# Performance work log

Measured on AMD Instinct MI355X. Metric: run time of the kernel, lower is better.

The kernel has to match this reference:

```python
import jax, jax.numpy as jnp
import numpy as np

VOCAB, E, H, OUT = 50000, 300, 512, 256
D = 2 * H  # bidirectional
B, T = 64, 256
EPS = 1e-5


def setup_inputs() -> dict:
    key = jax.random.key(0)
    ks = jax.random.split(key, 16)
    s = 0.05
    inp = {
        'inputs': jax.random.randint(ks[0], (B, T), 0, VOCAB, dtype=jnp.int32),
        'mask': jnp.zeros((B, T), dtype=bool),
        'embed_table': jax.random.normal(ks[1], (VOCAB, E), jnp.float32) * s,
        # forward-direction LSTM (PyTorch gate order i,f,g,o)
        'w_ih_f': jax.random.normal(ks[2], (4 * H, E), jnp.float32) * s,
        'w_hh_f': jax.random.normal(ks[3], (4 * H, H), jnp.float32) * s,
        'b_ih_f': jax.random.normal(ks[4], (4 * H,), jnp.float32) * s,
        'b_hh_f': jax.random.normal(ks[5], (4 * H,), jnp.float32) * s,
        # backward-direction LSTM
        'w_ih_b': jax.random.normal(ks[6], (4 * H, E), jnp.float32) * s,
        'w_hh_b': jax.random.normal(ks[7], (4 * H, H), jnp.float32) * s,
        'b_ih_b': jax.random.normal(ks[8], (4 * H,), jnp.float32) * s,
        'b_hh_b': jax.random.normal(ks[9], (4 * H,), jnp.float32) * s,
        # SoftDotAttention
        'w_in': jax.random.normal(ks[10], (D, D), jnp.float32) * s,       # linear_in, no bias
        'w_out_attn': jax.random.normal(ks[11], (D, 2 * D), jnp.float32) * s,  # linear_out, no bias
        # output head + BatchNorm affine
        'w_out': jax.random.normal(ks[12], (OUT, D), jnp.float32) * s,
        'b_out': jax.random.normal(ks[13], (OUT,), jnp.float32) * s,
        'gamma': jnp.ones((OUT,), jnp.float32),
        'beta': jnp.zeros((OUT,), jnp.float32),
    }
    return inp


def _lstm_dir(x, w_ih, w_hh, b_ih, b_hh, reverse):
    # x: [B, T, E] -> hs: [B, T, H]
    bsz = x.shape[0]
    h0 = jnp.zeros((bsz, w_hh.shape[1]), x.dtype)
    c0 = jnp.zeros_like(h0)
    x_pre = jnp.einsum('bte,ge->btg', x, w_ih) + (b_ih + b_hh)  # precompute input proj

    def cell(carry, xt):
        h, c = carry
        gates = xt + h @ w_hh.T
        i, f, g, o = jnp.split(gates, 4, axis=-1)
        i, f, o = jax.nn.sigmoid(i), jax.nn.sigmoid(f), jax.nn.sigmoid(o)
        g = jnp.tanh(g)
        c = f * c + i * g
        h = o * jnp.tanh(c)
        return (h, c), h

    _, hs = jax.lax.scan(cell, (h0, c0), jnp.swapaxes(x_pre, 0, 1), reverse=reverse)
    return jnp.swapaxes(hs, 0, 1)


def reference(inputs, mask, embed_table, w_ih_f, w_hh_f, b_ih_f, b_hh_f,
              w_ih_b, w_hh_b, b_ih_b, b_hh_b, w_in, w_out_attn,
              w_out, b_out, gamma, beta):
    embeds = embed_table[inputs]                       # [B,T,E]; dropout = identity (eval)
    h_f = _lstm_dir(embeds, w_ih_f, w_hh_f, b_ih_f, b_hh_f, reverse=False)
    h_b = _lstm_dir(embeds, w_ih_b, w_hh_b, b_ih_b, b_hh_b, reverse=True)
    ctx = jnp.concatenate([h_f, h_b], axis=-1)         # [B,T,D]

    # vectorized SoftDotAttention over all query timesteps (the original Python loop)
    target = jnp.einsum('bqd,ed->bqe', ctx, w_in)      # linear_in(ctx[:,q])
    scores = jnp.einsum('bqd,bkd->bqk', target, ctx)   # [B,T,T]
    scores = jnp.where(mask[:, None, :], -jnp.inf, scores)
    attn = jax.nn.softmax(scores, axis=-1)
    weighted = jnp.einsum('bqk,bkd->bqd', attn, ctx)   # [B,T,D]
    h_tilde = jnp.tanh(jnp.einsum('bqc,dc->bqd',
                                  jnp.concatenate([weighted, ctx], axis=-1),
                                  w_out_attn))          # [B,T,D]

    ctx_out = jnp.mean(h_tilde, axis=1)                # [B,D]
    y = jnp.tanh(ctx_out @ w_out.T + b_out)            # [B,OUT]

    # BatchNorm1d, training-mode batch statistics (biased variance)
    mu = jnp.mean(y, axis=0)
    var = jnp.mean((y - mu) ** 2, axis=0)
    out = gamma * (y - mu) * jax.lax.rsqrt(var + EPS) + beta
    return out
```

## Files before the change

kernel.cpp:

```cpp
#include <hip/hip_runtime.h>
#include <hip/hip_fp16.h>

#define NB   64
#define NT   256
#define NE   300
#define NH   512
#define ND   1024
#define NOUT 256

typedef _Float16 f16;
typedef _Float16 f16x4 __attribute__((ext_vector_type(4)));
typedef _Float16 f16x8 __attribute__((ext_vector_type(8)));
typedef float    f32x4 __attribute__((ext_vector_type(4)));

static __device__ __forceinline__ float sigmoidf_(float x) {
  return 1.f / (1.f + __expf(-x));
}
static __device__ __forceinline__ float tanhf_(float x) {
  return 1.f - 2.f / (__expf(2.f * x) + 1.f);
}

static __device__ __forceinline__ void gload16(const f16* g, f16* l) {
  __builtin_amdgcn_global_load_lds(
      (const __attribute__((address_space(1))) void*)g,
      (__attribute__((address_space(3))) void*)l, 16, 0, 0);
}

template <bool DUAL>
static __device__ __forceinline__ void mfma_tile128(
    const f16* __restrict__ A, const f16* __restrict__ A2,
    const f16* __restrict__ B, int K, int Ksplit, int ldA, int ldB,
    int m0, int n0, f32x4 acc[4][4], f16* As, f16* Bs)
{
  const int tid = threadIdx.x;
  const int lane = tid & 63, w = tid >> 6;
  const int wr = (w >> 1) * 64, wc = (w & 1) * 64;
  const int srow = w * 16 + (lane >> 2);
  const int scol = (lane & 3) * 8;
  const f16* A0  = A + (size_t)(m0 + srow) * ldA + scol;
  const f16* A1  = A + (size_t)(m0 + 64 + srow) * ldA + scol;
  const f16* A20 = DUAL ? (A2 + (size_t)(m0 + srow) * ldA + scol) : A0;
  const f16* A21 = DUAL ? (A2 + (size_t)(m0 + 64 + srow) * ldA + scol) : A1;
  const f16* B0  = B + (size_t)(n0 + srow) * ldB + scol;
  const f16* B1  = B + (size_t)(n0 + 64 + srow) * ldB + scol;
  f16* Asw0 = As + w * 512;
  f16* Asw1 = As + 2048 + w * 512;
  f16* Bsw0 = Bs + w * 512;
  f16* Bsw1 = Bs + 2048 + w * 512;
  for (int kt = 0; kt < K; kt += 32) {
    if (!DUAL || kt < Ksplit) {
      gload16(A0 + kt, Asw0);
      gload16(A1 + kt, Asw1);
    } else {
      gload16(A20 + (kt - Ksplit), Asw0);
      gload16(A21 + (kt - Ksplit), Asw1);
    }
    gload16(B0 + kt, Bsw0);
    gload16(B1 + kt, Bsw1);
    __syncthreads();
    f16x8 af[4], bf[4];
#pragma unroll
    for (int i = 0; i < 4; ++i) {
      af[i] = *(const f16x8*)&As[(wr + i * 16 + (lane & 15)) * 32 + (lane >> 4) * 8];
      bf[i] = *(const f16x8*)&Bs[(wc + i * 16 + (lane & 15)) * 32 + (lane >> 4) * 8];
    }
#pragma unroll
    for (int i = 0; i < 4; ++i)
#pragma unroll
      for (int j = 0; j < 4; ++j)
        acc[i][j] = __builtin_amdgcn_mfma_f32_16x16x32_f16(
            af[i], bf[j], acc[i][j], 0, 0, 0);
    __syncthreads();
  }
}

__global__ __launch_bounds__(256) void gemm128_h2h(
    const f16* __restrict__ A, const f16* __restrict__ B, f16* __restrict__ C,
    int N, int K, int sA, int sB, int sC)
{
  __shared__ __align__(16) f16 As[4096], Bs[4096];
  const f16* Ab = A + (size_t)blockIdx.z * sA;
  const f16* Bb = B + (size_t)blockIdx.z * sB;
  f16*       Cb = C + (size_t)blockIdx.z * sC;
  const int m0 = blockIdx.y * 128, n0 = blockIdx.x * 128;
  f32x4 acc[4][4] = {};
  mfma_tile128<false>(Ab, Ab, Bb, K, K, K, K, m0, n0, acc, As, Bs);
  const int lane = threadIdx.x & 63, w = threadIdx.x >> 6;
  const int wr = (w >> 1) * 64, wc = (w & 1) * 64;
#pragma unroll
  for (int i = 0; i < 4; ++i) {
    const int row = m0 + wr + i * 16 + (lane >> 4) * 4;
#pragma unroll
    for (int j = 0; j < 4; ++j) {
      const int col = n0 + wc + j * 16 + (lane & 15);
#pragma unroll
      for (int r = 0; r < 4; ++r)
        Cb[(size_t)(row + r) * N + col] = (f16)acc[i][j][r];
    }
  }
}

__global__ __launch_bounds__(256) void gemm128_h2f(
    const f16* __restrict__ A, const f16* __restrict__ B, float* __restrict__ C,
    int N, int K, int sA, int sB, int sC)
{
  __shared__ __align__(16) f16 As[4096], Bs[4096];
  const f16* Ab = A + (size_t)blockIdx.z * sA;
  const f16* Bb = B + (size_t)blockIdx.z * sB;
  float*     Cb = C + (size_t)blockIdx.z * sC;
  const int m0 = blockIdx.y * 128, n0 = blockIdx.x * 128;
  f32x4 acc[4][4] = {};
  mfma_tile128<false>(Ab, Ab, Bb, K, K, K, K, m0, n0, acc, As, Bs);
  const int lane = threadIdx.x & 63, w = threadIdx.x >> 6;
  const int wr = (w >> 1) * 64, wc = (w & 1) * 64;
#pragma unroll
  for (int i = 0; i < 4; ++i) {
    const int row = m0 + wr + i * 16 + (lane >> 4) * 4;
#pragma unroll
    for (int j = 0; j < 4; ++j) {
      const int col = n0 + wc + j * 16 + (lane & 15);
#pragma unroll
      for (int r = 0; r < 4; ++r)
        Cb[(size_t)(row + r) * N + col] = acc[i][j][r];
    }
  }
}

__global__ __launch_bounds__(256) void xpre_mfma(
    const f16* __restrict__ A, const f16* __restrict__ B,
    const float* __restrict__ bihf, const float* __restrict__ bhhf,
    const float* __restrict__ bihb, const float* __restrict__ bhhb,
    f16* __restrict__ xq)
{
  __shared__ __align__(16) f16 As[2048], Bs[2048];
  __shared__ __align__(16) f16 ldsT[64 * 72];
  __shared__ float biasS[64];
  const int ds = blockIdx.x;
  const int dir = ds >> 5, slice = ds & 31;
  const int t0 = blockIdx.y;
  const int tid = threadIdx.x, lane = tid & 63, w = tid >> 6;
  if (tid < 64) {
    int row = dir * 2048 + (tid & 3) * 512 + slice * 16 + (tid >> 2);
    biasS[tid] = (row < 2048) ? (bihf[row] + bhhf[row])
                              : (bihb[row - 2048] + bhhb[row - 2048]);
  }
  const int srow = w * 16 + (lane >> 2);
  const int scol = (lane & 3) * 8;
  const f16* Ab = A + ((size_t)(srow * 256 + t0)) * 320 + scol;
  const int brow = dir * 2048 + (srow & 3) * 512 + slice * 16 + (srow >> 2);
  const f16* Bb = B + (size_t)brow * 320 + scol;
  f16* Asw = As + w * 512;
  f16* Bsw = Bs + w * 512;
  f32x4 acc[4] = {};
  for (int kt = 0; kt < 320; kt += 32) {
    gload16(Ab + kt, Asw);
    gload16(Bb + kt, Bsw);
    __syncthreads();
    f16x8 a = *(const f16x8*)&As[(w * 16 + (lane & 15)) * 32 + (lane >> 4) * 8];
#pragma unroll
    for (int j = 0; j < 4; ++j) {
      f16x8 b = *(const f16x8*)&Bs[(j * 16 + (lane & 15)) * 32 + (lane >> 4) * 8];
      acc[j] = __builtin_amdgcn_mfma_f32_16x16x32_f16(a, b, acc[j], 0, 0, 0);
    }
    __syncthreads();
  }
#pragma unroll
  for (int j = 0; j < 4; ++j) {
    const int cl = j * 16 + (lane & 15);
#pragma unroll
    for (int r = 0; r < 4; ++r) {
      int b = w * 16 + (lane >> 4) * 4 + r;
      ldsT[b * 72 + cl] = (f16)(acc[j][r] + biasS[cl]);
    }
  }
  __syncthreads();
  f16* base = xq + (((size_t)t0 * 2 + dir) * 32 + slice) * 4096;
#pragma unroll
  for (int p = 0; p < 2; ++p) {
    int e = tid + 256 * p;
    int b = e >> 3, q8 = (e & 7) * 8;
    *(uint4*)(base + b * 64 + q8) = *(const uint4*)&ldsT[b * 72 + q8];
  }
}

__global__ __launch_bounds__(256) void htilde_mfma(
    const f16* __restrict__ Wt, const f16* __restrict__ CTX,
    const f16* __restrict__ Wo, float* __restrict__ ctx_out)
{
  __shared__ __align__(16) f16 As[4096], Bs[4096];
  __shared__ float red[4][128];
  const int m0 = blockIdx.y * 128, n0 = blockIdx.x * 128;
  f32x4 acc[4][4] = {};
  mfma_tile128<true>(Wt, CTX, Wo, 2048, 1024, 1024, 2048, m0, n0, acc, As, Bs);
  const int lane = threadIdx.x & 63, w = threadIdx.x >> 6;
  const int wc = (w & 1) * 64;
#pragma unroll
  for (int j = 0; j < 4; ++j) {
    float s = 0.f;
#pragma unroll
    for (int i = 0; i < 4; ++i)
#pragma unroll
      for (int r = 0; r < 4; ++r) s += tanhf(acc[i][j][r]);
    s += __shfl_xor(s, 16, 64);
    s += __shfl_xor(s, 32, 64);
    if (lane < 16) red[w][wc + j * 16 + lane] = s;
  }
  __syncthreads();
  if (threadIdx.x < 128) {
    const int col = threadIdx.x;
    float s = (col < 64) ? (red[0][col] + red[2][col])
                         : (red[1][col] + red[3][col]);
    int b = m0 >> 8;
    atomicAdd(&ctx_out[(size_t)b * ND + n0 + col], s);
  }
}

__global__ __launch_bounds__(256, 1) void lstm_persist(
    const f16* __restrict__ xq, const float* __restrict__ whhf,
    const float* __restrict__ whhb, f16* __restrict__ hseq)
{
  __shared__ __align__(16) f16 hx[2][64][24];
  const int blk = blockIdx.x;
  const int dir = blk >> 5;
  const int slice = blk & 31;
  const int j0 = slice * 16;
  const float* whh = dir ? whhb : whhf;
  const int tid = threadIdx.x, lane = tid & 63, w = tid >> 6;
  const int jj = lane & 15, ko = (lane >> 4) * 8;

  f16x8 bf[4][16];
#pragma unroll
  for (int g = 0; g < 4; ++g)
#pragma unroll
    for (int kt = 0; kt < 16; ++kt) {
      const float* src = whh + (size_t)(g * NH + j0 + jj) * NH + kt * 32 + ko;
      float4 u0 = *(const float4*)src;
      float4 u1 = *(const float4*)(src + 4);
      f16x8 v;
      v[0] = (f16)u0.x; v[1] = (f16)u0.y; v[2] = (f16)u0.z; v[3] = (f16)u0.w;
      v[4] = (f16)u1.x; v[5] = (f16)u1.y; v[6] = (f16)u1.z; v[7] = (f16)u1.w;
      bf[g][kt] = v;
    }

  float c[4] = {0.f, 0.f, 0.f, 0.f};
  const int eb = tid >> 2, eg = tid & 3;
  const int aoff = (ko >> 4) * 1024 + (w * 16 + jj) * 16 + (ko & 8);

  float xg[4][4];
  auto ldxg = [&](int t) {
    const int tl = dir ? (NT - 1 - t) : t;
    const f16* base = xq + (((size_t)tl * 2 + dir) * 32 + slice) * 4096;
#pragma unroll
    for (int r = 0; r < 4; ++r) {
      const int b = w * 16 + (lane >> 4) * 4 + r;
      unsigned long long u = *(const unsigned long long*)(base + b * 64 + jj * 4);
      f16x4 x = __builtin_bit_cast(f16x4, u);
      xg[0][r] = (float)x[0];
      xg[1][r] = (float)x[1];
      xg[2][r] = (float)x[2];
      xg[3][r] = (float)x[3];
    }
  };
  ldxg(0);

  for (int t = 0; t < NT; ++t) {
    const int tt = dir ? (NT - 1 - t) : t;

    f32x4 acc[4] = {};
    if (t > 0) {
      const int ttp = dir ? (NT - t) : (t - 1);
      const f16* hp = hseq + ((size_t)ttp * 2 + dir) * 32768 + aoff;
      unsigned long long u0[16], u1[16];
#pragma unroll
      for (int kt = 0; kt < 16; ++kt) {
        u0[kt] = __hip_atomic_load(
            (const unsigned long long*)(hp + kt * 2048),
            __ATOMIC_RELAXED, __HIP_MEMORY_SCOPE_AGENT);
        u1[kt] = __hip_atomic_load(
            (const unsigned long long*)(hp + kt * 2048 + 4),
            __ATOMIC_RELAXED, __HIP_MEMORY_SCOPE_AGENT);
      }
      for (;;) {
        int nb = 0;
#pragma unroll
        for (int kt = 0; kt < 16; ++kt) {
          nb |= (unsigned)(u0[kt] >> 48) == 0xFFFFu;
          nb |= (unsigned)(u1[kt] >> 48) == 0xFFFFu;
        }
        if (!__any(nb)) break;
#pragma unroll
        for (int kt = 0; kt < 16; ++kt) {
          if ((unsigned)(u0[kt] >> 48) == 0xFFFFu)
            u0[kt] = __hip_atomic_load(
                (const unsigned long long*)(hp + kt * 2048),
                __ATOMIC_RELAXED, __HIP_MEMORY_SCOPE_AGENT);
          if ((unsigned)(u1[kt] >> 48) == 0xFFFFu)
            u1[kt] = __hip_atomic_load(
                (const unsigned long long*)(hp + kt * 2048 + 4),
                __ATOMIC_RELAXED, __HIP_MEMORY_SCOPE_AGENT);
        }
      }
#pragma unroll
      for (int kt = 0; kt < 16; ++kt) {
        f16x4 a0 = __builtin_bit_cast(f16x4, u0[kt]);
        f16x4 a1 = __builtin_bit_cast(f16x4, u1[kt]);
        f16x8 a = __builtin_shufflevector(a0, a1, 0, 1, 2, 3, 4, 5, 6, 7);
#pragma unroll
        for (int g = 0; g < 4; ++g)
          acc[g] = __builtin_amdgcn_mfma_f32_16x16x32_f16(a, bf[g][kt], acc[g], 0, 0, 0);
      }
    }
#pragma unroll
    for (int r = 0; r < 4; ++r) {
      float iv = sigmoidf_(acc[0][r] + xg[0][r]);
      float fv = sigmoidf_(acc[1][r] + xg[1][r]);
      float gv = tanhf_   (acc[2][r] + xg[2][r]);
      float ov = sigmoidf_(acc[3][r] + xg[3][r]);
      c[r] = fv * c[r] + iv * gv;
      float h = ov * tanhf_(c[r]);
      hx[t & 1][w * 16 + (lane >> 4) * 4 + r][jj] = (f16)h;
    }
    __syncthreads();
    f16x4 hv;
#pragma unroll
    for (int i = 0; i < 4; ++i) hv[i] = hx[t & 1][eb][eg * 4 + i];
    unsigned long long pu = __builtin_bit_cast(unsigned long long, hv);
    __hip_atomic_store(
        (unsigned long long*)(hseq + ((size_t)tt * 2 + dir) * 32768
                              + (size_t)slice * 1024 + eb * 16 + eg * 4),
        pu, __ATOMIC_RELAXED, __HIP_MEMORY_SCOPE_AGENT);
    if (t == NT - 1) break;
    ldxg(t + 1);
  }
}

__global__ __launch_bounds__(256) void fill_sent(unsigned long long* __restrict__ p)
{
  size_t i = (size_t)blockIdx.x * 1024 + threadIdx.x;
#pragma unroll
  for (int k = 0; k < 4; ++k)
    __hip_atomic_store(p + i + k * 256, 0xFFFFFFFFFFFFFFFFull,
                       __ATOMIC_RELAXED, __HIP_MEMORY_SCOPE_AGENT);
}

__global__ __launch_bounds__(256) void tr_k(
    const f16* __restrict__ hseq, f16* __restrict__ ctx, f16* __restrict__ ctxT)
{
  __shared__ __align__(16) f16 X[4][64][72];
  const int t0 = blockIdx.x * 64;
  const int dir = blockIdx.y;
  const int bg = blockIdx.z;
  const int tid = threadIdx.x;
  for (int ci = 0; ci < 8; ++ci) {
#pragma unroll
    for (int p = 0; p < 8; ++p) {
      int q = tid + 256 * p;
      int ti = q >> 5, rem = q & 31;
      int si = rem >> 3, s2 = rem & 7;
      int bi = s2 >> 1, jjh = (s2 & 1) * 8;
      const f16* src = hseq
          + (((size_t)(t0 + ti) * 2 + dir) * 32 + ci * 4 + si) * 1024
          + (bg * 4 + bi) * 16 + jjh;
      *(uint4*)&X[bi][ti][si * 16 + jjh] = *(const uint4*)src;
    }
    __syncthreads();
#pragma unroll
    for (int p = 0; p < 8; ++p) {
      int q = tid + 256 * p;
      int bi = q >> 9, rem = q & 511;
      int ti = rem >> 3, sub = (rem & 7) * 8;
      f16* dst = ctx + ((size_t)(bg * 4 + bi) * NT + t0 + ti) * ND
                 + dir * 512 + ci * 64 + sub;
      *(uint4*)dst = *(const uint4*)&X[bi][ti][sub];
    }
#pragma unroll
    for (int p = 0; p < 8; ++p) {
      int q = tid + 256 * p;
      int bi = q >> 9, rem = q & 511;
      int dl = rem >> 3, ts = (rem & 7) * 8;
      f16x8 v;
#pragma unroll
      for (int k = 0; k < 8; ++k) v[k] = X[bi][ts + k][dl];
      f16* dst = ctxT + ((size_t)(bg * 4 + bi) * ND + dir * 512 + ci * 64 + dl) * NT
                 + t0 + ts;
      *(f16x8*)dst = v;
    }
    __syncthreads();
  }
}

__global__ __launch_bounds__(256) void softmax_rows(
    const float* __restrict__ sc, f16* __restrict__ probs)
{
  const int row = blockIdx.x * 4 + (threadIdx.x >> 6);
  const int lane = threadIdx.x & 63;
  const float* p = sc + (size_t)row * NT;
  float4 v = *(const float4*)&p[lane * 4];
  float mx = fmaxf(fmaxf(v.x, v.y), fmaxf(v.z, v.w));
#pragma unroll
  for (int s = 32; s >= 1; s >>= 1) mx = fmaxf(mx, __shfl_xor(mx, s, 64));
  v.x = __expf(v.x - mx); v.y = __expf(v.y - mx);
  v.z = __expf(v.z - mx); v.w = __expf(v.w - mx);
  float sm = v.x + v.y + v.z + v.w;
#pragma unroll
  for (int s = 32; s >= 1; s >>= 1) sm += __shfl_xor(sm, s, 64);
  float inv = 1.f / sm;
  f16* q = probs + (size_t)row * NT + lane * 4;
  q[0] = (f16)(v.x * inv); q[1] = (f16)(v.y * inv);
  q[2] = (f16)(v.z * inv); q[3] = (f16)(v.w * inv);
}

__global__ __launch_bounds__(256) void head_k(
    const float* __restrict__ ctx_out, const float* __restrict__ w_out,
    const float* __restrict__ b_out, float* __restrict__ y)
{
  const int b = blockIdx.x;
  __shared__ float cl[ND];
#pragma unroll
  for (int l = 0; l < 4; ++l)
    cl[threadIdx.x + 256 * l] =
        ctx_out[(size_t)b * ND + threadIdx.x + 256 * l] * (1.f / (float)NT);
  __syncthreads();
  const int n = threadIdx.x;
  float acc = b_out[n];
  for (int k = 0; k < ND; k += 4) {
    float4 w = *(const float4*)&w_out[(size_t)n * ND + k];
    acc += cl[k] * w.x + cl[k + 1] * w.y + cl[k + 2] * w.z + cl[k + 3] * w.w;
  }
  y[b * NOUT + n] = tanhf(acc);
}

__global__ __launch_bounds__(64) void bn_k(
    const float* __restrict__ y, const float* __restrict__ gamma,
    const float* __restrict__ beta, float* __restrict__ out)
{
  const int n = blockIdx.x, b = threadIdx.x;
  float v = y[b * NOUT + n];
  float s = v, sq = v * v;
#pragma unroll
  for (int k = 32; k >= 1; k >>= 1) {
    s  += __shfl_xor(s, k, 64);
    sq += __shfl_xor(sq, k, 64);
  }
  float mu = s * (1.f / 64.f);
  float var = sq * (1.f / 64.f) - mu * mu;
  float r = rsqrtf(var + 1e-5f);
  out[b * NOUT + n] = gamma[n] * (v - mu) * r + beta[n];
}

__global__ __launch_bounds__(256) void zero_k(float4* __restrict__ p, int n4)
{
  int i = blockIdx.x * 256 + threadIdx.x;
  if (i < n4) p[i] = make_float4(0.f, 0.f, 0.f, 0.f);
}

__global__ __launch_bounds__(256) void gather_emb(
    const int* __restrict__ toks, const float* __restrict__ table,
    f16* __restrict__ emb)
{
  const int w = threadIdx.x >> 6, lane = threadIdx.x & 63;
  const int row = blockIdx.x * 4 + w;
  const int tok = toks[row];
  for (int k = lane; k < 320; k += 64)
    emb[(size_t)row * 320 + k] = (k < NE) ? (f16)table[(size_t)tok * NE + k]
                                          : (f16)0.f;
}

__global__ __launch_bounds__(256) void cvt_wih(
    const float* __restrict__ wf, const float* __restrict__ wb,
    f16* __restrict__ o)
{
  const int row = blockIdx.x;
  const float* src = (row < 2048) ? (wf + (size_t)row * NE)
                                  : (wb + (size_t)(row - 2048) * NE);
  for (int k = threadIdx.x; k < 320; k += 256)
    o[(size_t)row * 320 + k] = (k < NE) ? (f16)src[k] : (f16)0.f;
}

__global__ __launch_bounds__(256) void cvt_flat(
    const float* __restrict__ in, f16* __restrict__ o, int n)
{
  int i = blockIdx.x * 256 + threadIdx.x;
  if (i < n) o[i] = (f16)in[i];
}

extern "C" void kernel_launch(void* const* d_in, const int* in_sizes, int n_in,
                              void* d_out, int out_size, void* d_ws,
                              size_t ws_size, hipStream_t stream)
{
  (void)in_sizes; (void)n_in; (void)out_size;
  const int*   inputs  = (const int*)d_in[0];
  const float* table   = (const float*)d_in[2];
  const float* w_ih_f  = (const float*)d_in[3];
  const float* w_hh_f  = (const float*)d_in[4];
  const float* b_ih_f  = (const float*)d_in[5];
  const float* b_hh_f  = (const float*)d_in[6];
  const float* w_ih_b  = (const float*)d_in[7];
  const float* w_hh_b  = (const float*)d_in[8];
  const float* b_ih_b  = (const float*)d_in[9];
  const float* b_hh_b  = (const float*)d_in[10];
  const float* w_in    = (const float*)d_in[11];
  const float* w_oattn = (const float*)d_in[12];
  const float* w_out   = (const float*)d_in[13];
  const float* b_out   = (const float*)d_in[14];
  const float* gamma   = (const float*)d_in[15];
  const float* beta    = (const float*)d_in[16];

  char* ws = (char*)d_ws;
  f16*   xq      = (f16*)ws;
  f16*   ctxT_h  = (f16*)ws;
  f16*   tw_h    = (f16*)(ws + 33554432);
  float* scores  = (float*)(ws + 67108864);
  f16*   probs   = (f16*)(ws + 83886080);
  f16*   w_in_h  = (f16*)(ws + 92274688);
  f16*   ctx_h   = (f16*)(ws + 134217728);
  f16*   hseq    = (f16*)(ws + 167772160);
  f16*   emb_h   = (f16*)(ws + 201326592);
  float* ctxout  = (float*)(ws + 201588736);
  float* yb      = (float*)(ws + 201850880);
  f16*   wih_h   = (f16*)(ws + 211812352);
  f16*   w_oattn_h = (f16*)(ws + 214433792);
  if (ws_size < 218628096ULL) return;

  gather_emb<<<4096, 256, 0, stream>>>(inputs, table, emb_h);
  cvt_wih<<<4096, 256, 0, stream>>>(w_ih_f, w_ih_b, wih_h);
  cvt_flat<<<8192, 256, 0, stream>>>(w_oattn, w_oattn_h, 2097152);

  fill_sent<<<4096, 256, 0, stream>>>((unsigned long long*)hseq);

  xpre_mfma<<<dim3(64, 256), 256, 0, stream>>>(
      emb_h, wih_h, b_ih_f, b_hh_f, b_ih_b, b_hh_b, xq);

  zero_k<<<82, 256, 0, stream>>>((float4*)ctxout, 20992);
  lstm_persist<<<64, 256, 0, stream>>>(xq, w_hh_f, w_hh_b, hseq);

  tr_k<<<dim3(4, 2, 16), 256, 0, stream>>>(hseq, ctx_h, ctxT_h);

  cvt_flat<<<4096, 256, 0, stream>>>(w_in, w_in_h, 1048576);
  gemm128_h2h<<<dim3(8, 128, 1), 256, 0, stream>>>(
      ctx_h, w_in_h, tw_h, ND, ND, 0, 0, 0);

  gemm128_h2f<<<dim3(2, 2, NB), 256, 0, stream>>>(
      tw_h, ctx_h, scores, NT, ND, NT * ND, NT * ND, NT * NT);

  softmax_rows<<<(NB * NT) / 4, 256, 0, stream>>>(scores, probs);

  gemm128_h2h<<<dim3(8, 2, NB), 256, 0, stream>>>(
      probs, ctxT_h, tw_h, ND, NT, NT * NT, ND * NT, NT * ND);

  htilde_mfma<<<dim3(8, 128), 256, 0, stream>>>(tw_h, ctx_h, w_oattn_h, ctxout);

  head_k<<<NB, 256, 0, stream>>>(ctxout, w_out, b_out, yb);

  bn_k<<<NOUT, 64, 0, stream>>>(yb, gamma, beta, (float*)d_out);
}
```

Measured before the change: 1.559 ms.

## Enlarge xpre GEMM tile to 128x128 and merge prep kernels into one launch

The input-projection GEMM now gives each block two timesteps and two gate slices, a 128x128 tile, with a 4x4 MFMA accumulator per wave instead of 1x4. Each loaded operand fragment is reused across more MFMAs and the grid shrinks fourfold. Separately, the embedding gather, weight conversions and sentinel fill are fused into one prep kernel to cut launch overhead. The larger tile raises register and LDS use, which may lower occupancy.

```diff
diff --git a/kernel.cpp b/kernel.cpp
--- a/kernel.cpp
+++ b/kernel.cpp
@@ -132,54 +132,76 @@
     const float* __restrict__ bihb, const float* __restrict__ bhhb,
     f16* __restrict__ xq)
 {
-  __shared__ __align__(16) f16 As[2048], Bs[2048];
-  __shared__ __align__(16) f16 ldsT[64 * 72];
-  __shared__ float biasS[64];
-  const int ds = blockIdx.x;
-  const int dir = ds >> 5, slice = ds & 31;
-  const int t0 = blockIdx.y;
+  __shared__ __align__(16) f16 As[4096], Bs[4096];
+  __shared__ __align__(16) f16 ldsT[4][64][72];
+  __shared__ float biasS[128];
+  const int bx = blockIdx.x;
+  const int dir = bx >> 4, sp = bx & 15;
+  const int by = blockIdx.y;
   const int tid = threadIdx.x, lane = tid & 63, w = tid >> 6;
-  if (tid < 64) {
-    int row = dir * 2048 + (tid & 3) * 512 + slice * 16 + (tid >> 2);
-    biasS[tid] = (row < 2048) ? (bihf[row] + bhhf[row])
-                              : (bihb[row - 2048] + bhhb[row - 2048]);
-  }
-  const int srow = w * 16 + (lane >> 2);
+  if (tid < 128) {
+    int nc = tid & 63, soff = tid >> 6;
+    int rr = (nc & 3) * 512 + (sp * 2 + soff) * 16 + (nc >> 2);
+    biasS[tid] = dir ? (bihb[rr] + bhhb[rr]) : (bihf[rr] + bhhf[rr]);
+  }
+  const int s0 = w * 16 + (lane >> 2);
   const int scol = (lane & 3) * 8;
-  const f16* Ab = A + ((size_t)(srow * 256 + t0)) * 320 + scol;
-  const int brow = dir * 2048 + (srow & 3) * 512 + slice * 16 + (srow >> 2);
-  const f16* Bb = B + (size_t)brow * 320 + scol;
-  f16* Asw = As + w * 512;
-  f16* Bsw = Bs + w * 512;
-  f32x4 acc[4] = {};
+  const f16* A0 = A + ((size_t)s0 * 256 + 2 * by) * 320 + scol;
+  const f16* A1 = A0 + 320;
+  const int brow0 = dir * 2048 + (s0 & 3) * 512 + (sp * 2 + 0) * 16 + (s0 >> 2);
+  const int brow1 = dir * 2048 + (s0 & 3) * 512 + (sp * 2 + 1) * 16 + (s0 >> 2);
+  const f16* B0 = B + (size_t)brow0 * 320 + scol;
+  const f16* B1 = B + (size_t)brow1 * 320 + scol;
+  f16* Asw0 = As + w * 512;  f16* Asw1 = As + 2048 + w * 512;
+  f16* Bsw0 = Bs + w * 512;  f16* Bsw1 = Bs + 2048 + w * 512;
+  const int wr = (w >> 1) * 64, wc = (w & 1) * 64;
+  f32x4 acc[4][4] = {};
   for (int kt = 0; kt < 320; kt += 32) {
-    gload16(Ab + kt, Asw);
-    gload16(Bb + kt, Bsw);
-    __syncthreads();
-    f16x8 a = *(const f16x8*)&As[(w * 16 + (lane & 15)) * 32 + (lane >> 4) * 8];
-#pragma unroll
-    for (int j = 0; j < 4; ++j) {
-      f16x8 b = *(const f16x8*)&Bs[(j * 16 + (lane & 15)) * 32 + (lane >> 4) * 8];
-      acc[j] = __builtin_amdgcn_mfma_f32_16x16x32_f16(a, b, acc[j], 0, 0, 0);
-    }
+    gload16(A0 + kt, Asw0);
+    gload16(A1 + kt, Asw1);
+    gload16(B0 + kt, Bsw0);
+    gload16(B1 + kt, Bsw1);
+    __syncthreads();
+    f16x8 af[4], bf[4];
+#pragma unroll
+    for (int i = 0; i < 4; ++i) {
+      af[i] = *(const f16x8*)&As[(wr + i * 16 + (lane & 15)) * 32 + (lane >> 4) * 8];
+      bf[i] = *(const f16x8*)&Bs[(wc + i * 16 + (lane & 15)) * 32 + (lane >> 4) * 8];
+    }
+#pragma unroll
+    for (int i = 0; i < 4; ++i)
+#pragma unroll
+      for (int j = 0; j < 4; ++j)
+        acc[i][j] = __builtin_amdgcn_mfma_f32_16x16x32_f16(
+            af[i], bf[j], acc[i][j], 0, 0, 0);
     __syncthreads();
   }
 #pragma unroll
   for (int j = 0; j < 4; ++j) {
-    const int cl = j * 16 + (lane & 15);
-#pragma unroll
-    for (int r = 0; r < 4; ++r) {
-      int b = w * 16 + (lane >> 4) * 4 + r;
-      ldsT[b * 72 + cl] = (f16)(acc[j][r] + biasS[cl]);
+    const int n = wc + j * 16 + (lane & 15);
+    const int soff = n >> 6, nc = n & 63;
+    const float bias = biasS[n];
+#pragma unroll
+    for (int i = 0; i < 4; ++i) {
+#pragma unroll
+      for (int r = 0; r < 4; ++r) {
+        int row = wr + i * 16 + (lane >> 4) * 4 + r;
+        int dt = row >> 6, b = row & 63;
+        ldsT[dt * 2 + soff][b][nc] = (f16)(acc[i][j][r] + bias);
+      }
     }
   }
   __syncthreads();
-  f16* base = xq + (((size_t)t0 * 2 + dir) * 32 + slice) * 4096;
-#pragma unroll
-  for (int p = 0; p < 2; ++p) {
-    int e = tid + 256 * p;
-    int b = e >> 3, q8 = (e & 7) * 8;
-    *(uint4*)(base + b * 64 + q8) = *(const uint4*)&ldsT[b * 72 + q8];
+#pragma unroll
+  for (int sl = 0; sl < 4; ++sl) {
+    const int dt = sl >> 1, soff = sl & 1;
+    f16* base = xq + (((size_t)(2 * by + dt) * 2 + dir) * 32 + (sp * 2 + soff)) * 4096;
+#pragma unroll
+    for (int p = 0; p < 2; ++p) {
+      int e = tid + 256 * p;
+      int b = e >> 3, q8 = (e & 7) * 8;
+      *(uint4*)(base + b * 64 + q8) = *(const uint4*)&ldsT[sl][b][q8];
+    }
   }
 }
 
@@ -334,13 +356,61 @@
   }
 }
 
-__global__ __launch_bounds__(256) void fill_sent(unsigned long long* __restrict__ p)
-{
-  size_t i = (size_t)blockIdx.x * 1024 + threadIdx.x;
-#pragma unroll
-  for (int k = 0; k < 4; ++k)
-    __hip_atomic_store(p + i + k * 256, 0xFFFFFFFFFFFFFFFFull,
-                       __ATOMIC_RELAXED, __HIP_MEMORY_SCOPE_AGENT);
+__global__ __launch_bounds__(256) void prep_k(
+    const int* __restrict__ toks, const float* __restrict__ table,
+    f16* __restrict__ emb,
+    const float* __restrict__ wf, const float* __restrict__ wb,
+    f16* __restrict__ wih,
+    const float* __restrict__ woa, f16* __restrict__ woa_h,
+    unsigned long long* __restrict__ sent)
+{
+  int bb = blockIdx.x;
+  const int tid = threadIdx.x;
+  if (bb < 4096) {
+    const int w = tid >> 6, lane = tid & 63;
+    const int row = bb * 4 + w;
+    const int tok = toks[row];
+    for (int k = lane; k < 320; k += 64)
+      emb[(size_t)row * 320 + k] = (k < NE) ? (f16)table[(size_t)tok * NE + k]
+                                            : (f16)0.f;
+    return;
+  }
+  bb -= 4096;
+  if (bb < 4096) {
+    const int row = bb;
+    const float* src = (row < 2048) ? (wf + (size_t)row * NE)
+                                    : (wb + (size_t)(row - 2048) * NE);
+    for (int k = tid; k < 320; k += 256)
+      wih[(size_t)row * 320 + k] = (k < NE) ? (f16)src[k] : (f16)0.f;
+    return;
+  }
+  bb -= 4096;
+  if (bb < 8192) {
+    int i = bb * 256 + tid;
+    woa_h[i] = (f16)woa[i];
+    return;
+  }
+  bb -= 8192;
+  {
+    size_t i = (size_t)bb * 1024 + tid;
+#pragma unroll
+    for (int k = 0; k < 4; ++k)
+      __hip_atomic_store(sent + i + k * 256, 0xFFFFFFFFFFFFFFFFull,
+                         __ATOMIC_RELAXED, __HIP_MEMORY_SCOPE_AGENT);
+  }
+}
+
+__global__ __launch_bounds__(256) void zero_k(float4* __restrict__ p, int n4)
+{
+  int i = blockIdx.x * 256 + threadIdx.x;
+  if (i < n4) p[i] = make_float4(0.f, 0.f, 0.f, 0.f);
+}
+
+__global__ __launch_bounds__(256) void cvt_flat(
+    const float* __restrict__ in, f16* __restrict__ o, int n)
+{
+  int i = blockIdx.x * 256 + threadIdx.x;
+  if (i < n) o[i] = (f16)in[i];
 }
 
 __global__ __launch_bounds__(256) void tr_k(
@@ -446,42 +516,6 @@
   float var = sq * (1.f / 64.f) - mu * mu;
   float r = rsqrtf(var + 1e-5f);
   out[b * NOUT + n] = gamma[n] * (v - mu) * r + beta[n];
-}
-
-__global__ __launch_bounds__(256) void zero_k(float4* __restrict__ p, int n4)
-{
-  int i = blockIdx.x * 256 + threadIdx.x;
-  if (i < n4) p[i] = make_float4(0.f, 0.f, 0.f, 0.f);
-}
-
-__global__ __launch_bounds__(256) void gather_emb(
-    const int* __restrict__ toks, const float* __restrict__ table,
-    f16* __restrict__ emb)
-{
-  const int w = threadIdx.x >> 6, lane = threadIdx.x & 63;
-  const int row = blockIdx.x * 4 + w;
-  const int tok = toks[row];
-  for (int k = lane; k < 320; k += 64)
-    emb[(size_t)row * 320 + k] = (k < NE) ? (f16)table[(size_t)tok * NE + k]
-                                          : (f16)0.f;
-}
-
-__global__ __launch_bounds__(256) void cvt_wih(
-    const float* __restrict__ wf, const float* __restrict__ wb,
-    f16* __restrict__ o)
-{
-  const int row = blockIdx.x;
-  const float* src = (row < 2048) ? (wf + (size_t)row * NE)
-                                  : (wb + (size_t)(row - 2048) * NE);
-  for (int k = threadIdx.x; k < 320; k += 256)
-    o[(size_t)row * 320 + k] = (k < NE) ? (f16)src[k] : (f16)0.f;
-}
-
-__global__ __launch_bounds__(256) void cvt_flat(
-    const float* __restrict__ in, f16* __restrict__ o, int n)
-{
-  int i = blockIdx.x * 256 + threadIdx.x;
-  if (i < n) o[i] = (f16)in[i];
 }
 
 extern "C" void kernel_launch(void* const* d_in, const int* in_sizes, int n_in,
@@ -522,13 +556,11 @@
   f16*   w_oattn_h = (f16*)(ws + 214433792);
   if (ws_size < 218628096ULL) return;
 
-  gather_emb<<<4096, 256, 0, stream>>>(inputs, table, emb_h);
-  cvt_wih<<<4096, 256, 0, stream>>>(w_ih_f, w_ih_b, wih_h);
-  cvt_flat<<<8192, 256, 0, stream>>>(w_oattn, w_oattn_h, 2097152);
-
-  fill_sent<<<4096, 256, 0, stream>>>((unsigned long long*)hseq);
-
-  xpre_mfma<<<dim3(64, 256), 256, 0, stream>>>(
+  prep_k<<<20480, 256, 0, stream>>>(
+      inputs, table, emb_h, w_ih_f, w_ih_b, wih_h,
+      w_oattn, w_oattn_h, (unsigned long long*)hseq);
+
+  xpre_mfma<<<dim3(32, 128), 256, 0, stream>>>(
       emb_h, wih_h, b_ih_f, b_hh_f, b_ih_b, b_hh_b, xq);
 
   zero_k<<<82, 256, 0, stream>>>((float4*)ctxout, 20992);
```

After: 1.529 ms, median of 2. No clear change (-1.9%).
